# Kernel optimization log

Measured on AMD Instinct MI355X. Metric: run time of the kernel, lower is better.

Reference implementation:

```python
import jax, jax.numpy as jnp
import numpy as np

B, S, HH, WW = 256, 384, 12, 16
D = HH * WW          # 192, LSTM input dim
H = 100              # hidden_dim
C = 250              # output_dim (N_CLASSES)


def setup_inputs() -> dict:
    key = jax.random.key(0)
    k1, k2, k3, k4 = jax.random.split(key, 4)
    x = jax.random.normal(k1, (B, S, HH, WW), dtype=jnp.float32)
    # Glorot-ish scaling to keep the recurrence numerically tame
    W = jax.random.normal(k2, (D, 4 * H), dtype=jnp.float32) / np.sqrt(D)
    U = jax.random.normal(k3, (H, 4 * H), dtype=jnp.float32) / np.sqrt(H)
    b = jnp.zeros((4 * H,), dtype=jnp.float32)
    Wd = jax.random.normal(k4, (H, C), dtype=jnp.float32) / np.sqrt(H)
    bd = jnp.zeros((C,), dtype=jnp.float32)
    return {"x": x, "W": W, "U": U, "b": b, "Wd": Wd, "bd": bd}


def _lstm_last_hidden(x3, W, U, b):
    # x3: [B, S, D]. Keras gate order: i, f, c(g), o.
    pre = jnp.einsum('bsd,dk->sbk', x3, W) + b  # time-major [S, B, 4H]
    h0 = jnp.zeros((x3.shape[0], H), dtype=x3.dtype)
    c0 = jnp.zeros_like(h0)

    def step(carry, xt):
        h, c = carry
        z = xt + h @ U                      # [B, 4H]
        i = jax.nn.sigmoid(z[:, 0 * H:1 * H])
        f = jax.nn.sigmoid(z[:, 1 * H:2 * H])
        g = jnp.tanh(z[:, 2 * H:3 * H])
        o = jax.nn.sigmoid(z[:, 3 * H:4 * H])
        c_new = f * c + i * g
        h_new = o * jnp.tanh(c_new)
        return (h_new, c_new), None

    (hT, _), _ = jax.lax.scan(step, (h0, c0), pre)
    return hT  # [B, H] == out[:, -1, :] since return_sequences last step = final state


def reference(x, W, U, b, Wd, bd):
    b_, s_, hh_, ww_ = x.shape
    x3 = x.reshape(b_, s_, hh_ * ww_)
    hT = _lstm_last_hidden(x3, W, U, b)
    # Dropout layers are identity at inference (training=False)
    return hT @ Wd + bd  # [B, C] logits
```

## Files before the change

kernel.cpp:

```cpp
#include <hip/hip_runtime.h>
#include <cstdint>
#include <cstddef>

#define S_LEN 384
#define BATCH 256
#define DIM   192
#define HID   100
#define G4    400
#define NCLS  250

#define WSTEPS 16
#define NWIN   24
#define NTILES 28
#define NKC    6

#define LOG2E  1.4426950408889634f
#define LOG2E2 2.8853900817779268f

typedef float    f32x4   __attribute__((ext_vector_type(4)));
typedef short    bf16x8  __attribute__((ext_vector_type(8)));
typedef _Float16 half2_t __attribute__((ext_vector_type(2)));
typedef _Float16 f16x4   __attribute__((ext_vector_type(4)));
typedef _Float16 f16x8   __attribute__((ext_vector_type(8)));

static __device__ __forceinline__ unsigned short f2bf(float f) {
    unsigned u = __float_as_uint(f);
    return (unsigned short)((u + 0x7FFFu + ((u >> 16) & 1u)) >> 16);
}

static __device__ __forceinline__ unsigned cvtpk(float a, float b) {
    unsigned r;
    asm("v_cvt_pk_bf16_f32 %0, %1, %2" : "=v"(r) : "v"(a), "v"(b));
    return r;
}

template<int CTRL>
static __device__ __forceinline__ float fdpp(float x) {
    return __int_as_float(
        __builtin_amdgcn_mov_dpp(__float_as_int(x), CTRL, 0xF, 0xF, true));
}
#define DPP_X1 0xB1
#define DPP_X2 0x4E
#define DPP_B0 0x00
#define DPP_B1 0x55
#define DPP_B2 0xAA
#define DPP_B3 0xFF

__global__ void prep(const float* __restrict__ W, const float* __restrict__ U,
                     unsigned short* __restrict__ Wf, half2_t* __restrict__ Ut4)
{
    int bid = blockIdx.x;
    if (bid < 336) {
        int i = bid * 256 + threadIdx.x;
        int e    = i & 7;
        int fi   = i >> 3;
        int lane = fi & 63;
        int ck   = fi >> 6;
        int ct   = ck / 6, kc = ck - ct * 6;
        int m    = lane & 15, q = lane >> 4;
        int gate = ct / 7, jj = ct - gate * 7;
        int unit = jj * 16 + m;
        int d    = kc * 32 + q * 8 + e;
        float v  = (unit < HID) ? W[(size_t)d * G4 + gate * HID + unit] : 0.0f;
        Wf[i] = f2bf(v);
    } else {
        int i = (bid - 336) * 256 + threadIdx.x;
        if (i >= 20800) return;
        int n    = i / 208;
        int rem  = i - n * 208;
        int q    = rem / 52;
        int rem2 = rem - q * 52;
        int mm   = rem2 / 13;
        int r    = rem2 - mm * 13;
        int col  = (q ^ mm) * HID + n;
        int j0   = 26 * q + 2 * r;
        half2_t v;
        v.x = (_Float16)(j0     < HID ? U[(size_t)j0       * G4 + col] : 0.0f);
        v.y = (_Float16)(j0 + 1 < HID ? U[(size_t)(j0 + 1) * G4 + col] : 0.0f);
        Ut4[i] = v;
    }
}

__global__ __launch_bounds__(512)
__attribute__((amdgpu_waves_per_eu(2, 2)))
void scan_fused(const float* __restrict__ x, const unsigned short* __restrict__ Wf,
                const half2_t* __restrict__ Ut4, const float* __restrict__ bias,
                const float* __restrict__ Wd, const float* __restrict__ bd,
                float* __restrict__ out)
{
    __shared__ __align__(16) _Float16 h2[2][4][40];
    __shared__ __align__(16) float hf32[HID];
    __shared__ __align__(16) _Float16 zbuf[2][448 * WSTEPS];

    const int b  = blockIdx.x;
    const int t  = threadIdx.x;

    const int q  = t & 3;
    const int nr = t >> 2;
    const bool active = (nr < HID);
    const int n  = active ? nr : HID - 1;
    const int wq = n / 26, wi = n - wq * 26;

    const int lane = t & 63;
    const int w    = t >> 6;
    const int m    = lane & 15;
    const int q4   = lane >> 4;
    const int ntile = (w < 4) ? 4 : 3;
    const int tbase = (w < 4) ? (w * 4) : (16 + (w - 4) * 3);

    float bv[4];
#pragma unroll
    for (int i = 0; i < 4; ++i) {
        int ct   = tbase + i;
        int gate = ct / 7, jj = ct - gate * 7;
        int unit = jj * 16 + m;
        bv[i] = (i < ntile && unit < HID) ? bias[gate * HID + unit] : 0.0f;
    }

    const float* __restrict__ xb = x + (size_t)b * S_LEN * DIM;
    float4 xv[NKC][2];

#define LOADX(S0)                                                             \
    { int xr = (S0) + m;                                                      \
      _Pragma("unroll")                                                       \
      for (int kc = 0; kc < NKC; ++kc) {                                      \
          const float* p = xb + (size_t)xr * DIM + kc * 32 + q4 * 8;          \
          xv[kc][0] = *(const float4*)p;                                      \
          xv[kc][1] = *(const float4*)(p + 4);                                \
      } }

#define PRODUCE(NB)                                                           \
    { bf16x8 Af[NKC];                                                         \
      _Pragma("unroll")                                                       \
      for (int kc = 0; kc < NKC; ++kc) {                                      \
          int4 ai;                                                            \
          ai.x = (int)cvtpk(xv[kc][0].x, xv[kc][0].y);                        \
          ai.y = (int)cvtpk(xv[kc][0].z, xv[kc][0].w);                        \
          ai.z = (int)cvtpk(xv[kc][1].x, xv[kc][1].y);                        \
          ai.w = (int)cvtpk(xv[kc][1].z, xv[kc][1].w);                        \
          Af[kc] = *(bf16x8*)&ai;                                             \
      }                                                                       \
      _Pragma("unroll")                                                       \
      for (int i = 0; i < 4; ++i) if (i < ntile) {                            \
          int ct = tbase + i;                                                 \
          const unsigned short* bp = Wf + ((size_t)ct * NKC * 64 + lane) * 8; \
          f32x4 acc = {bv[i], bv[i], bv[i], bv[i]};                           \
          _Pragma("unroll")                                                   \
          for (int kc = 0; kc < NKC; ++kc) {                                  \
              bf16x8 Bf = *(const bf16x8*)(bp + (size_t)kc * 512);            \
              acc = __builtin_amdgcn_mfma_f32_16x16x32_bf16(Af[kc], Bf, acc, 0, 0, 0); \
          }                                                                   \
          f16x4 zq;                                                           \
          zq[0] = (_Float16)acc[0]; zq[1] = (_Float16)acc[1];                 \
          zq[2] = (_Float16)acc[2]; zq[3] = (_Float16)acc[3];                 \
          *(f16x4*)&zbuf[NB][(ct * 16 + m) * WSTEPS + q4 * 4] = zq;           \
      } }

    half2_t Uc[4][13];
#pragma unroll
    for (int mm = 0; mm < 4; ++mm) {
        const half2_t* up = Ut4 + (size_t)((n * 4 + q) * 4 + mm) * 13;
#pragma unroll
        for (int r = 0; r < 13; ++r) Uc[mm][r] = up[r];
    }

    if (t < 320) ((_Float16*)h2)[t] = (_Float16)0.f;
    float c = 0.f;

    LOADX(0);
    PRODUCE(0);
    LOADX(WSTEPS);
    __syncthreads();

    const float scale = (q == 2) ? -LOG2E2 : -LOG2E;
    const float Aact  = (q == 2) ? 2.0f : 1.0f;
    const float Bact  = (q == 2) ? -1.0f : 0.0f;

    float hn_last = 0.f;

    auto step = [&](float zk, int cur) {
        const _Float16* hb = &h2[cur][q][0];
        f16x8   g0 = *(const f16x8*)(hb);
        f16x8   g1 = *(const f16x8*)(hb + 8);
        f16x8   g2 = *(const f16x8*)(hb + 16);
        half2_t g3 = *(const half2_t*)(hb + 24);
        half2_t hp[13];
        hp[0]  = __builtin_shufflevector(g0, g0, 0, 1);
        hp[1]  = __builtin_shufflevector(g0, g0, 2, 3);
        hp[2]  = __builtin_shufflevector(g0, g0, 4, 5);
        hp[3]  = __builtin_shufflevector(g0, g0, 6, 7);
        hp[4]  = __builtin_shufflevector(g1, g1, 0, 1);
        hp[5]  = __builtin_shufflevector(g1, g1, 2, 3);
        hp[6]  = __builtin_shufflevector(g1, g1, 4, 5);
        hp[7]  = __builtin_shufflevector(g1, g1, 6, 7);
        hp[8]  = __builtin_shufflevector(g2, g2, 0, 1);
        hp[9]  = __builtin_shufflevector(g2, g2, 2, 3);
        hp[10] = __builtin_shufflevector(g2, g2, 4, 5);
        hp[11] = __builtin_shufflevector(g2, g2, 6, 7);
        hp[12] = g3;

        float p0 = 0.f, p1 = 0.f, p2 = 0.f, p3 = 0.f;
#pragma unroll
        for (int r = 0; r < 13; ++r) {
            p0 = __builtin_amdgcn_fdot2(Uc[0][r], hp[r], p0, false);
            p1 = __builtin_amdgcn_fdot2(Uc[1][r], hp[r], p1, false);
            p2 = __builtin_amdgcn_fdot2(Uc[2][r], hp[r], p2, false);
            p3 = __builtin_amdgcn_fdot2(Uc[3][r], hp[r], p3, false);
        }
        float s0 = p0 + fdpp<DPP_X1>(p1);
        float s2 = p2 + fdpp<DPP_X1>(p3);
        float a  = s0 + fdpp<DPP_X2>(s2) + zk;

        float v = fmaf(Aact,
                       __builtin_amdgcn_rcpf(1.0f + __builtin_amdgcn_exp2f(scale * a)),
                       Bact);

        float bi = fdpp<DPP_B0>(v);
        float bf = fdpp<DPP_B1>(v);
        float bg = fdpp<DPP_B2>(v);
        float bo = fdpp<DPP_B3>(v);

        c = fmaf(bf, c, bi * bg);
        float tc = fmaf(2.0f,
                        __builtin_amdgcn_rcpf(1.0f + __builtin_amdgcn_exp2f(-LOG2E2 * c)),
                        -1.0f);
        float hn = bo * tc;
        if (q == 0 && active) h2[cur ^ 1][wq][wi] = (_Float16)hn;
        hn_last = hn;
        __syncthreads();
    };

    const int col = q * 112 + n;

    for (int j = 0; j < NWIN; ++j) {
        f16x8 zA = *(const f16x8*)&zbuf[j & 1][col * WSTEPS];
        f16x8 zB = *(const f16x8*)&zbuf[j & 1][col * WSTEPS + 8];
        if (j < NWIN - 1) PRODUCE((j + 1) & 1);
        if (j < NWIN - 2) LOADX((j + 2) * WSTEPS);
#pragma unroll
        for (int k = 0; k < 8; ++k) step((float)zA[k], k & 1);
#pragma unroll
        for (int k = 0; k < 8; ++k) step((float)zB[k], k & 1);
    }

    if (q == 0 && active) hf32[n] = hn_last;
    __syncthreads();
    if (t < NCLS) {
        float acc2 = bd[t];
        const float4* h4 = (const float4*)hf32;
#pragma unroll 5
        for (int j4 = 0; j4 < 25; ++j4) {
            float4 hv = h4[j4];
            acc2 = fmaf(hv.x, Wd[(size_t)(4 * j4 + 0) * NCLS + t], acc2);
            acc2 = fmaf(hv.y, Wd[(size_t)(4 * j4 + 1) * NCLS + t], acc2);
            acc2 = fmaf(hv.z, Wd[(size_t)(4 * j4 + 2) * NCLS + t], acc2);
            acc2 = fmaf(hv.w, Wd[(size_t)(4 * j4 + 3) * NCLS + t], acc2);
        }
        out[(size_t)b * NCLS + t] = acc2;
    }
}

extern "C" void kernel_launch(void* const* d_in, const int* in_sizes, int n_in,
                              void* d_out, int out_size, void* d_ws, size_t ws_size,
                              hipStream_t stream)
{
    const float* x    = (const float*)d_in[0];
    const float* W    = (const float*)d_in[1];
    const float* U    = (const float*)d_in[2];
    const float* bias = (const float*)d_in[3];
    const float* Wd   = (const float*)d_in[4];
    const float* bd   = (const float*)d_in[5];
    float* out = (float*)d_out;

    unsigned int* wsb = (unsigned int*)d_ws;
    unsigned short* Wf  = (unsigned short*)wsb;
    half2_t*        Ut4 = (half2_t*)(wsb + 43008);

    prep<<<418, 256, 0, stream>>>(W, U, Wf, Ut4);
    scan_fused<<<BATCH, 512, 0, stream>>>(x, Wf, Ut4, bias, Wd, bd, out);
}
```

Before: 314.2 us.

## Dedicate one wave to input projection and spread tile production across steps

Wave 7 now produces the x·W input projection alone. It spreads the 28 MFMA tiles of the next window over the 16 recurrence steps, one or two tiles per barrier. Waves 0-6 run only the serial LSTM recurrence and the final dense layer. Previously every wave ran a burst of MFMA and conversion work at the start of each window, inside the serial chain. Bias is now pre-laid-out per tile in the prep kernel. The risk is that the single producer wave, including its global loads of W tiles, takes longer than one recurrence step and holds up the shared barriers.

```diff
diff --git a/kernel.cpp b/kernel.cpp
--- a/kernel.cpp
+++ b/kernel.cpp
@@ -47,7 +47,9 @@
 #define DPP_B3 0xFF
 
 __global__ void prep(const float* __restrict__ W, const float* __restrict__ U,
-                     unsigned short* __restrict__ Wf, half2_t* __restrict__ Ut4)
+                     const float* __restrict__ bias,
+                     unsigned short* __restrict__ Wf, float* __restrict__ biasf,
+                     half2_t* __restrict__ Ut4)
 {
     int bid = blockIdx.x;
     if (bid < 336) {
@@ -65,26 +67,34 @@
         Wf[i] = f2bf(v);
     } else {
         int i = (bid - 336) * 256 + threadIdx.x;
-        if (i >= 20800) return;
-        int n    = i / 208;
-        int rem  = i - n * 208;
-        int q    = rem / 52;
-        int rem2 = rem - q * 52;
-        int mm   = rem2 / 13;
-        int r    = rem2 - mm * 13;
-        int col  = (q ^ mm) * HID + n;
-        int j0   = 26 * q + 2 * r;
-        half2_t v;
-        v.x = (_Float16)(j0     < HID ? U[(size_t)j0       * G4 + col] : 0.0f);
-        v.y = (_Float16)(j0 + 1 < HID ? U[(size_t)(j0 + 1) * G4 + col] : 0.0f);
-        Ut4[i] = v;
+        if (i < 448) {
+            int ct = i >> 4, mm = i & 15;
+            int gate = ct / 7, jj = ct - gate * 7;
+            int unit = jj * 16 + mm;
+            biasf[i] = (unit < HID) ? bias[gate * HID + unit] : 0.0f;
+        } else {
+            int i2 = i - 448;
+            if (i2 >= 20800) return;
+            int n    = i2 / 208;
+            int rem  = i2 - n * 208;
+            int q    = rem / 52;
+            int rem2 = rem - q * 52;
+            int mm   = rem2 / 13;
+            int r    = rem2 - mm * 13;
+            int col  = (q ^ mm) * HID + n;
+            int j0   = 26 * q + 2 * r;
+            half2_t v;
+            v.x = (_Float16)(j0     < HID ? U[(size_t)j0       * G4 + col] : 0.0f);
+            v.y = (_Float16)(j0 + 1 < HID ? U[(size_t)(j0 + 1) * G4 + col] : 0.0f);
+            Ut4[i2] = v;
+        }
     }
 }
 
 __global__ __launch_bounds__(512)
 __attribute__((amdgpu_waves_per_eu(2, 2)))
 void scan_fused(const float* __restrict__ x, const unsigned short* __restrict__ Wf,
-                const half2_t* __restrict__ Ut4, const float* __restrict__ bias,
+                const half2_t* __restrict__ Ut4, const float* __restrict__ biasf,
                 const float* __restrict__ Wd, const float* __restrict__ bd,
                 float* __restrict__ out)
 {
@@ -92,171 +102,180 @@
     __shared__ __align__(16) float hf32[HID];
     __shared__ __align__(16) _Float16 zbuf[2][448 * WSTEPS];
 
-    const int b  = blockIdx.x;
-    const int t  = threadIdx.x;
-
-    const int q  = t & 3;
-    const int nr = t >> 2;
-    const bool active = (nr < HID);
-    const int n  = active ? nr : HID - 1;
-    const int wq = n / 26, wi = n - wq * 26;
-
+    const int b    = blockIdx.x;
+    const int t    = threadIdx.x;
     const int lane = t & 63;
     const int w    = t >> 6;
-    const int m    = lane & 15;
-    const int q4   = lane >> 4;
-    const int ntile = (w < 4) ? 4 : 3;
-    const int tbase = (w < 4) ? (w * 4) : (16 + (w - 4) * 3);
-
-    float bv[4];
-#pragma unroll
-    for (int i = 0; i < 4; ++i) {
-        int ct   = tbase + i;
-        int gate = ct / 7, jj = ct - gate * 7;
-        int unit = jj * 16 + m;
-        bv[i] = (i < ntile && unit < HID) ? bias[gate * HID + unit] : 0.0f;
-    }
-
-    const float* __restrict__ xb = x + (size_t)b * S_LEN * DIM;
-    float4 xv[NKC][2];
-
-#define LOADX(S0)                                                             \
-    { int xr = (S0) + m;                                                      \
-      _Pragma("unroll")                                                       \
-      for (int kc = 0; kc < NKC; ++kc) {                                      \
-          const float* p = xb + (size_t)xr * DIM + kc * 32 + q4 * 8;          \
-          xv[kc][0] = *(const float4*)p;                                      \
-          xv[kc][1] = *(const float4*)(p + 4);                                \
-      } }
-
-#define PRODUCE(NB)                                                           \
-    { bf16x8 Af[NKC];                                                         \
-      _Pragma("unroll")                                                       \
-      for (int kc = 0; kc < NKC; ++kc) {                                      \
-          int4 ai;                                                            \
-          ai.x = (int)cvtpk(xv[kc][0].x, xv[kc][0].y);                        \
-          ai.y = (int)cvtpk(xv[kc][0].z, xv[kc][0].w);                        \
-          ai.z = (int)cvtpk(xv[kc][1].x, xv[kc][1].y);                        \
-          ai.w = (int)cvtpk(xv[kc][1].z, xv[kc][1].w);                        \
-          Af[kc] = *(bf16x8*)&ai;                                             \
-      }                                                                       \
-      _Pragma("unroll")                                                       \
-      for (int i = 0; i < 4; ++i) if (i < ntile) {                            \
-          int ct = tbase + i;                                                 \
-          const unsigned short* bp = Wf + ((size_t)ct * NKC * 64 + lane) * 8; \
-          f32x4 acc = {bv[i], bv[i], bv[i], bv[i]};                           \
-          _Pragma("unroll")                                                   \
-          for (int kc = 0; kc < NKC; ++kc) {                                  \
-              bf16x8 Bf = *(const bf16x8*)(bp + (size_t)kc * 512);            \
-              acc = __builtin_amdgcn_mfma_f32_16x16x32_bf16(Af[kc], Bf, acc, 0, 0, 0); \
-          }                                                                   \
-          f16x4 zq;                                                           \
-          zq[0] = (_Float16)acc[0]; zq[1] = (_Float16)acc[1];                 \
-          zq[2] = (_Float16)acc[2]; zq[3] = (_Float16)acc[3];                 \
-          *(f16x4*)&zbuf[NB][(ct * 16 + m) * WSTEPS + q4 * 4] = zq;           \
-      } }
-
-    half2_t Uc[4][13];
-#pragma unroll
-    for (int mm = 0; mm < 4; ++mm) {
-        const half2_t* up = Ut4 + (size_t)((n * 4 + q) * 4 + mm) * 13;
-#pragma unroll
-        for (int r = 0; r < 13; ++r) Uc[mm][r] = up[r];
-    }
 
     if (t < 320) ((_Float16*)h2)[t] = (_Float16)0.f;
-    float c = 0.f;
-
-    LOADX(0);
-    PRODUCE(0);
-    LOADX(WSTEPS);
-    __syncthreads();
-
-    const float scale = (q == 2) ? -LOG2E2 : -LOG2E;
-    const float Aact  = (q == 2) ? 2.0f : 1.0f;
-    const float Bact  = (q == 2) ? -1.0f : 0.0f;
-
-    float hn_last = 0.f;
-
-    auto step = [&](float zk, int cur) {
-        const _Float16* hb = &h2[cur][q][0];
-        f16x8   g0 = *(const f16x8*)(hb);
-        f16x8   g1 = *(const f16x8*)(hb + 8);
-        f16x8   g2 = *(const f16x8*)(hb + 16);
-        half2_t g3 = *(const half2_t*)(hb + 24);
-        half2_t hp[13];
-        hp[0]  = __builtin_shufflevector(g0, g0, 0, 1);
-        hp[1]  = __builtin_shufflevector(g0, g0, 2, 3);
-        hp[2]  = __builtin_shufflevector(g0, g0, 4, 5);
-        hp[3]  = __builtin_shufflevector(g0, g0, 6, 7);
-        hp[4]  = __builtin_shufflevector(g1, g1, 0, 1);
-        hp[5]  = __builtin_shufflevector(g1, g1, 2, 3);
-        hp[6]  = __builtin_shufflevector(g1, g1, 4, 5);
-        hp[7]  = __builtin_shufflevector(g1, g1, 6, 7);
-        hp[8]  = __builtin_shufflevector(g2, g2, 0, 1);
-        hp[9]  = __builtin_shufflevector(g2, g2, 2, 3);
-        hp[10] = __builtin_shufflevector(g2, g2, 4, 5);
-        hp[11] = __builtin_shufflevector(g2, g2, 6, 7);
-        hp[12] = g3;
-
-        float p0 = 0.f, p1 = 0.f, p2 = 0.f, p3 = 0.f;
-#pragma unroll
-        for (int r = 0; r < 13; ++r) {
-            p0 = __builtin_amdgcn_fdot2(Uc[0][r], hp[r], p0, false);
-            p1 = __builtin_amdgcn_fdot2(Uc[1][r], hp[r], p1, false);
-            p2 = __builtin_amdgcn_fdot2(Uc[2][r], hp[r], p2, false);
-            p3 = __builtin_amdgcn_fdot2(Uc[3][r], hp[r], p3, false);
-        }
-        float s0 = p0 + fdpp<DPP_X1>(p1);
-        float s2 = p2 + fdpp<DPP_X1>(p3);
-        float a  = s0 + fdpp<DPP_X2>(s2) + zk;
-
-        float v = fmaf(Aact,
-                       __builtin_amdgcn_rcpf(1.0f + __builtin_amdgcn_exp2f(scale * a)),
-                       Bact);
-
-        float bi = fdpp<DPP_B0>(v);
-        float bf = fdpp<DPP_B1>(v);
-        float bg = fdpp<DPP_B2>(v);
-        float bo = fdpp<DPP_B3>(v);
-
-        c = fmaf(bf, c, bi * bg);
-        float tc = fmaf(2.0f,
-                        __builtin_amdgcn_rcpf(1.0f + __builtin_amdgcn_exp2f(-LOG2E2 * c)),
-                        -1.0f);
-        float hn = bo * tc;
-        if (q == 0 && active) h2[cur ^ 1][wq][wi] = (_Float16)hn;
-        hn_last = hn;
+
+    if (w == 7) {
+        const int pm = lane & 15;
+        const int pq = lane >> 4;
+        const float* __restrict__ xb = x + (size_t)b * S_LEN * DIM;
+        float4 xv[NKC][2];
+        bf16x8 Af[NKC];
+
+        auto loadx = [&](int s0) {
+            int xr = s0 + pm;
+#pragma unroll
+            for (int kc = 0; kc < NKC; ++kc) {
+                const float* p = xb + (size_t)xr * DIM + kc * 32 + pq * 8;
+                xv[kc][0] = *(const float4*)p;
+                xv[kc][1] = *(const float4*)(p + 4);
+            }
+        };
+        auto cvt = [&]() {
+#pragma unroll
+            for (int kc = 0; kc < NKC; ++kc) {
+                int4 ai;
+                ai.x = (int)cvtpk(xv[kc][0].x, xv[kc][0].y);
+                ai.y = (int)cvtpk(xv[kc][0].z, xv[kc][0].w);
+                ai.z = (int)cvtpk(xv[kc][1].x, xv[kc][1].y);
+                ai.w = (int)cvtpk(xv[kc][1].z, xv[kc][1].w);
+                Af[kc] = *(bf16x8*)&ai;
+            }
+        };
+        auto ptile = [&](int ct, int nb) {
+            float bvv = biasf[ct * 16 + pm];
+            const unsigned short* bp = Wf + ((size_t)ct * (NKC * 64) + lane) * 8;
+            f32x4 acc = {0.f, 0.f, 0.f, 0.f};
+#pragma unroll
+            for (int kc = 0; kc < NKC; ++kc) {
+                bf16x8 Bf = *(const bf16x8*)(bp + (size_t)kc * 512);
+                acc = __builtin_amdgcn_mfma_f32_16x16x32_bf16(Af[kc], Bf, acc, 0, 0, 0);
+            }
+            f16x4 zq;
+            zq[0] = (_Float16)(acc[0] + bvv);
+            zq[1] = (_Float16)(acc[1] + bvv);
+            zq[2] = (_Float16)(acc[2] + bvv);
+            zq[3] = (_Float16)(acc[3] + bvv);
+            *(f16x4*)&zbuf[nb][(ct * 16 + pm) * WSTEPS + pq * 4] = zq;
+        };
+
+        loadx(0);
+        cvt();
+        for (int ct = 0; ct < NTILES; ++ct) ptile(ct, 0);
+        loadx(WSTEPS);
         __syncthreads();
-    };
-
-    const int col = q * 112 + n;
-
-    for (int j = 0; j < NWIN; ++j) {
-        f16x8 zA = *(const f16x8*)&zbuf[j & 1][col * WSTEPS];
-        f16x8 zB = *(const f16x8*)&zbuf[j & 1][col * WSTEPS + 8];
-        if (j < NWIN - 1) PRODUCE((j + 1) & 1);
-        if (j < NWIN - 2) LOADX((j + 2) * WSTEPS);
-#pragma unroll
-        for (int k = 0; k < 8; ++k) step((float)zA[k], k & 1);
-#pragma unroll
-        for (int k = 0; k < 8; ++k) step((float)zB[k], k & 1);
-    }
-
-    if (q == 0 && active) hf32[n] = hn_last;
-    __syncthreads();
-    if (t < NCLS) {
-        float acc2 = bd[t];
-        const float4* h4 = (const float4*)hf32;
+
+        for (int j = 0; j < NWIN; ++j) {
+            const bool hasNext = (j < NWIN - 1);
+            if (hasNext) cvt();
+            if (j < NWIN - 2) loadx((j + 2) * WSTEPS);
+            const int nb = (j + 1) & 1;
+#pragma unroll 1
+            for (int k = 0; k < WSTEPS; ++k) {
+                if (hasNext) {
+                    ptile(k, nb);
+                    if (k < NTILES - WSTEPS) ptile(WSTEPS + k, nb);
+                }
+                __syncthreads();
+            }
+        }
+        __syncthreads();
+    } else {
+        const int q  = t & 3;
+        const int nr = t >> 2;
+        const bool active = (nr < HID);
+        const int n  = active ? nr : HID - 1;
+        const int wq = n / 26, wi = n - wq * 26;
+
+        half2_t Uc[4][13];
+#pragma unroll
+        for (int mm = 0; mm < 4; ++mm) {
+            const half2_t* up = Ut4 + (size_t)((n * 4 + q) * 4 + mm) * 13;
+#pragma unroll
+            for (int r = 0; r < 13; ++r) Uc[mm][r] = up[r];
+        }
+
+        float c = 0.f;
+        __syncthreads();
+
+        const float scale = (q == 2) ? -LOG2E2 : -LOG2E;
+        const float Aact  = (q == 2) ? 2.0f : 1.0f;
+        const float Bact  = (q == 2) ? -1.0f : 0.0f;
+
+        float hn_last = 0.f;
+
+        auto step = [&](float zk, int cur) {
+            const _Float16* hb = &h2[cur][q][0];
+            f16x8   g0 = *(const f16x8*)(hb);
+            f16x8   g1 = *(const f16x8*)(hb + 8);
+            f16x8   g2 = *(const f16x8*)(hb + 16);
+            half2_t g3 = *(const half2_t*)(hb + 24);
+            half2_t hp[13];
+            hp[0]  = __builtin_shufflevector(g0, g0, 0, 1);
+            hp[1]  = __builtin_shufflevector(g0, g0, 2, 3);
+            hp[2]  = __builtin_shufflevector(g0, g0, 4, 5);
+            hp[3]  = __builtin_shufflevector(g0, g0, 6, 7);
+            hp[4]  = __builtin_shufflevector(g1, g1, 0, 1);
+            hp[5]  = __builtin_shufflevector(g1, g1, 2, 3);
+            hp[6]  = __builtin_shufflevector(g1, g1, 4, 5);
+            hp[7]  = __builtin_shufflevector(g1, g1, 6, 7);
+            hp[8]  = __builtin_shufflevector(g2, g2, 0, 1);
+            hp[9]  = __builtin_shufflevector(g2, g2, 2, 3);
+            hp[10] = __builtin_shufflevector(g2, g2, 4, 5);
+            hp[11] = __builtin_shufflevector(g2, g2, 6, 7);
+            hp[12] = g3;
+
+            float p0 = 0.f, p1 = 0.f, p2 = 0.f, p3 = 0.f;
+#pragma unroll
+            for (int r = 0; r < 13; ++r) {
+                p0 = __builtin_amdgcn_fdot2(Uc[0][r], hp[r], p0, false);
+                p1 = __builtin_amdgcn_fdot2(Uc[1][r], hp[r], p1, false);
+                p2 = __builtin_amdgcn_fdot2(Uc[2][r], hp[r], p2, false);
+                p3 = __builtin_amdgcn_fdot2(Uc[3][r], hp[r], p3, false);
+            }
+            float s0 = p0 + fdpp<DPP_X1>(p1);
+            float s2 = p2 + fdpp<DPP_X1>(p3);
+            float a  = s0 + fdpp<DPP_X2>(s2) + zk;
+
+            float v = fmaf(Aact,
+                           __builtin_amdgcn_rcpf(1.0f + __builtin_amdgcn_exp2f(scale * a)),
+                           Bact);
+
+            float bi = fdpp<DPP_B0>(v);
+            float bf = fdpp<DPP_B1>(v);
+            float bg = fdpp<DPP_B2>(v);
+            float bo = fdpp<DPP_B3>(v);
+
+            c = fmaf(bf, c, bi * bg);
+            float tc = fmaf(2.0f,
+                            __builtin_amdgcn_rcpf(1.0f + __builtin_amdgcn_exp2f(-LOG2E2 * c)),
+                            -1.0f);
+            float hn = bo * tc;
+            if (q == 0 && active) h2[cur ^ 1][wq][wi] = (_Float16)hn;
+            hn_last = hn;
+            __syncthreads();
+        };
+
+        const int col = q * 112 + n;
+
+        for (int j = 0; j < NWIN; ++j) {
+            f16x8 zA = *(const f16x8*)&zbuf[j & 1][col * WSTEPS];
+            f16x8 zB = *(const f16x8*)&zbuf[j & 1][col * WSTEPS + 8];
+#pragma unroll
+            for (int k = 0; k < 8; ++k) step((float)zA[k], k & 1);
+#pragma unroll
+            for (int k = 0; k < 8; ++k) step((float)zB[k], k & 1);
+        }
+
+        if (q == 0 && active) hf32[n] = hn_last;
+        __syncthreads();
+        if (t < NCLS) {
+            float acc2 = bd[t];
+            const float4* h4 = (const float4*)hf32;
 #pragma unroll 5
-        for (int j4 = 0; j4 < 25; ++j4) {
-            float4 hv = h4[j4];
-            acc2 = fmaf(hv.x, Wd[(size_t)(4 * j4 + 0) * NCLS + t], acc2);
-            acc2 = fmaf(hv.y, Wd[(size_t)(4 * j4 + 1) * NCLS + t], acc2);
-            acc2 = fmaf(hv.z, Wd[(size_t)(4 * j4 + 2) * NCLS + t], acc2);
-            acc2 = fmaf(hv.w, Wd[(size_t)(4 * j4 + 3) * NCLS + t], acc2);
-        }
-        out[(size_t)b * NCLS + t] = acc2;
+            for (int j4 = 0; j4 < 25; ++j4) {
+                float4 hv = h4[j4];
+                acc2 = fmaf(hv.x, Wd[(size_t)(4 * j4 + 0) * NCLS + t], acc2);
+                acc2 = fmaf(hv.y, Wd[(size_t)(4 * j4 + 1) * NCLS + t], acc2);
+                acc2 = fmaf(hv.z, Wd[(size_t)(4 * j4 + 2) * NCLS + t], acc2);
+                acc2 = fmaf(hv.w, Wd[(size_t)(4 * j4 + 3) * NCLS + t], acc2);
+            }
+            out[(size_t)b * NCLS + t] = acc2;
+        }
     }
 }
 
@@ -273,9 +292,10 @@
     float* out = (float*)d_out;
 
     unsigned int* wsb = (unsigned int*)d_ws;
-    unsigned short* Wf  = (unsigned short*)wsb;
-    half2_t*        Ut4 = (half2_t*)(wsb + 43008);
-
-    prep<<<418, 256, 0, stream>>>(W, U, Wf, Ut4);
-    scan_fused<<<BATCH, 512, 0, stream>>>(x, Wf, Ut4, bias, Wd, bd, out);
-}
+    unsigned short* Wf    = (unsigned short*)wsb;
+    float*          biasf = (float*)(wsb + 43008);
+    half2_t*        Ut4   = (half2_t*)(wsb + 43456);
+
+    prep<<<419, 256, 0, stream>>>(W, U, bias, Wf, biasf, Ut4);
+    scan_fused<<<BATCH, 512, 0, stream>>>(x, Wf, Ut4, biasf, Wd, bd, out);
+}
```

New measurement: 353.9 us. 12.6% more time.
